# Optimization experiments

Measured on AMD Instinct MI355X. Metric: run time of the kernel, lower is better.

Reference implementation:

```python
import jax, jax.numpy as jnp
import numpy as np

N = 50000      # nodes
E = 800000     # edges (before self-loops)
IN_DIM = 128
HID = 64
OUT = 32
HEADS = 8
BN_EPS = 1e-5
NEG_SLOPE = 0.2  # PyG GATConv default


def setup_inputs() -> dict:
    key = jax.random.key(0)
    ks = jax.random.split(key, 24)
    g = lambda k, shape, fan_in: (jax.random.normal(k, shape, jnp.float32) / np.sqrt(fan_in))
    return {
        "x": jax.random.normal(ks[0], (N, IN_DIM), jnp.float32),
        "edge_index": jax.random.randint(ks[1], (2, E), 0, N, dtype=jnp.int64),
        # GCN1
        "gcn1_w": g(ks[2], (IN_DIM, HID), IN_DIM),
        "gcn1_b": jnp.zeros((HID,), jnp.float32),
        # BN1 (eval mode running stats)
        "bn1_gamma": jnp.ones((HID,), jnp.float32),
        "bn1_beta": jnp.zeros((HID,), jnp.float32),
        "bn1_mean": 0.1 * jax.random.normal(ks[3], (HID,), jnp.float32),
        "bn1_var": 0.5 + jax.random.uniform(ks[4], (HID,), jnp.float32),
        # GAT1: heads=8, per-head out=HID, concat=False -> mean over heads
        "gat1_w": g(ks[5], (HID, HEADS * HID), HID),
        "gat1_asrc": g(ks[6], (HEADS, HID), HID),
        "gat1_adst": g(ks[7], (HEADS, HID), HID),
        "gat1_b": jnp.zeros((HID,), jnp.float32),
        # GCN2
        "gcn2_w": g(ks[8], (HID, HID), HID),
        "gcn2_b": jnp.zeros((HID,), jnp.float32),
        # BN2
        "bn2_gamma": jnp.ones((HID,), jnp.float32),
        "bn2_beta": jnp.zeros((HID,), jnp.float32),
        "bn2_mean": 0.1 * jax.random.normal(ks[9], (HID,), jnp.float32),
        "bn2_var": 0.5 + jax.random.uniform(ks[10], (HID,), jnp.float32),
        # GAT2: heads=8, per-head out=OUT, concat=False
        "gat2_w": g(ks[11], (HID, HEADS * OUT), HID),
        "gat2_asrc": g(ks[12], (HEADS, OUT), OUT),
        "gat2_adst": g(ks[13], (HEADS, OUT), OUT),
        "gat2_b": jnp.zeros((OUT,), jnp.float32),
    }


def _gcn(x, src, dst, w, b, n):
    # PyG GCNConv: x @ W, symmetric norm with self-loops (src/dst already include them)
    h = x @ w
    deg = jax.ops.segment_sum(jnp.ones(src.shape[0], x.dtype), dst, num_segments=n)
    dinv = jnp.where(deg > 0, jax.lax.rsqrt(jnp.maximum(deg, 1.0)), 0.0)
    coef = dinv[src] * dinv[dst]                     # [E']
    out = jax.ops.segment_sum(coef[:, None] * h[src], dst, num_segments=n)
    return out + b


def _gat(x, src, dst, w, a_src, a_dst, b, n, heads, ch):
    # PyG GATConv (concat=False): mean over heads, softmax over incoming edges per dst
    h = (x @ w).reshape(n, heads, ch)                # [N,H,C]
    es = jnp.einsum('nhc,hc->nh', h, a_src)          # alpha_src per node
    ed = jnp.einsum('nhc,hc->nh', h, a_dst)
    e = jax.nn.leaky_relu(es[src] + ed[dst], NEG_SLOPE)  # [E',H]
    m = jax.ops.segment_max(e, dst, num_segments=n)
    m = jnp.where(jnp.isfinite(m), m, 0.0)
    ex = jnp.exp(e - m[dst])
    denom = jax.ops.segment_sum(ex, dst, num_segments=n)
    alpha = ex / (denom[dst] + 1e-16)                # [E',H]
    out = jnp.zeros((n, ch), x.dtype)
    for hd in range(heads):  # fixed small head loop keeps peak edge memory at [E',C]
        msg = alpha[:, hd, None] * h[src, hd]        # [E',C]
        out = out + jax.ops.segment_sum(msg, dst, num_segments=n)
    return out / heads + b


def _bn_eval(x, gamma, beta, mean, var):
    return (x - mean) * jax.lax.rsqrt(var + BN_EPS) * gamma + beta


def reference(x, edge_index,
              gcn1_w, gcn1_b, bn1_gamma, bn1_beta, bn1_mean, bn1_var,
              gat1_w, gat1_asrc, gat1_adst, gat1_b,
              gcn2_w, gcn2_b, bn2_gamma, bn2_beta, bn2_mean, bn2_var,
              gat2_w, gat2_asrc, gat2_adst, gat2_b):
    n = x.shape[0]
    loops = jnp.arange(n, dtype=edge_index.dtype)
    src = jnp.concatenate([edge_index[0], loops])    # self-loops (PyG default)
    dst = jnp.concatenate([edge_index[1], loops])

    h = _gcn(x, src, dst, gcn1_w, gcn1_b, n)
    h = jax.nn.relu(_bn_eval(h, bn1_gamma, bn1_beta, bn1_mean, bn1_var))
    h = jax.nn.relu(_gat(h, src, dst, gat1_w, gat1_asrc, gat1_adst, gat1_b, n, HEADS, HID))
    h = _gcn(h, src, dst, gcn2_w, gcn2_b, n)
    h = jax.nn.relu(_bn_eval(h, bn2_gamma, bn2_beta, bn2_mean, bn2_var))
    h = _gat(h, src, dst, gat2_w, gat2_asrc, gat2_adst, gat2_b, n, HEADS, OUT)
    return jax.nn.log_softmax(h, axis=1)
```

## Files before the change

### kernel.cpp

```cpp
#include <hip/hip_runtime.h>
#include <hip/hip_bf16.h>

#define NN 50000
#define NE 800000
#define IND 128
#define NH 8
#define EBLK 256
#define EPB 3125
#define NBUK 391
#define NBUKP 392
#define GH (NBUKP * EBLK)
#define PREPB 308

typedef __hip_bfloat16 bf16;
typedef __attribute__((ext_vector_type(8))) short short8;
typedef __attribute__((ext_vector_type(8))) __bf16 bf16x8;
typedef __attribute__((ext_vector_type(4))) float floatx4;
typedef __attribute__((ext_vector_type(2))) float floatx2;

static __device__ __forceinline__ short f2bf_bits(float f) {
    unsigned u = __float_as_uint(f);
    u = (u + 0x7fffu + ((u >> 16) & 1u)) >> 16;
    return (short)u;
}
static __device__ __forceinline__ float bf2f(bf16 v) { return __bfloat162float(v); }
static __device__ __forceinline__ floatx2 up2(unsigned av) {
    floatx2 r;
    r.x = __uint_as_float(av << 16);
    r.y = __uint_as_float(av & 0xffff0000u);
    return r;
}
static __device__ __forceinline__ unsigned pk2(float a, float b) {
    return (unsigned)(unsigned short)f2bf_bits(a) | ((unsigned)(unsigned short)f2bf_bits(b) << 16);
}

static __device__ __forceinline__ void scan_buckets(const int* __restrict__ bsum,
        int* sp, int* gb, int tid) {
    int v0 = (2 * tid < NBUKP) ? bsum[2 * tid] : 0;
    int v1 = (2 * tid + 1 < NBUKP) ? bsum[2 * tid + 1] : 0;
    int c = v0 + v1;
    sp[tid] = c; __syncthreads();
    int val = c;
#pragma unroll
    for (int off = 1; off < 256; off <<= 1) {
        int t = (tid >= off) ? sp[tid - off] : 0;
        __syncthreads();
        val += t; sp[tid] = val;
        __syncthreads();
    }
    int pex = val - c;
    gb[2 * tid] = pex;
    gb[2 * tid + 1] = pex + v0;
    __syncthreads();
}

__global__ __launch_bounds__(256) void bin_count_prep_kernel(const int* __restrict__ edst,
        int* __restrict__ ghist,
        const float* __restrict__ gcn1_w, const float* __restrict__ gcn2_w,
        const float* __restrict__ gat1_w, const float* __restrict__ gat2_w,
        const float* __restrict__ as1, const float* __restrict__ ad1,
        const float* __restrict__ as2, const float* __restrict__ ad2,
        bf16* __restrict__ wT1, bf16* __restrict__ wT2,
        bf16* __restrict__ wgT1, bf16* __restrict__ wgT2,
        float* __restrict__ was1, float* __restrict__ wad1,
        float* __restrict__ was2, float* __restrict__ wad2) {
    __shared__ int hsh[NBUKP];
    const int tid = threadIdx.x;
    if (blockIdx.x < EBLK) {
        const int blk = blockIdx.x;
        for (int b = tid; b < NBUKP; b += 256) hsh[b] = 0;
        __syncthreads();
        const int e0 = blk * EPB;
        for (int e = e0 + tid; e < e0 + EPB; e += 256)
            atomicAdd(&hsh[edst[e] >> 7], 1);
        __syncthreads();
        for (int b = tid; b < NBUKP; b += 256)
            ghist[b * EBLK + blk] = hsh[b];
    } else {
        int idx = (blockIdx.x - EBLK) * 256 + tid;
        if (idx < 8192) {
            int m = idx >> 7, k = idx & 127;
            ((short*)wT1)[idx] = f2bf_bits(gcn1_w[(long)k * 64 + m]);
        } else if (idx < 12288) {
            int i = idx - 8192;
            int m = i >> 6, k = i & 63;
            ((short*)wT2)[i] = f2bf_bits(gcn2_w[(long)k * 64 + m]);
        } else if (idx < 45056) {
            int i = idx - 12288;
            int m = i >> 9, k = i & 511;
            int h = k >> 6, c = k & 63;
            ((short*)wgT1)[i] = f2bf_bits(gat1_w[(long)c * 512 + h * 64 + m]);
        } else if (idx < 77824) {
            int i = idx - 45056;
            int m = i >> 9, k = i & 511;
            int h = k >> 6, c = k & 63;
            ((short*)wgT2)[i] = (m < 32) ? f2bf_bits(gat2_w[(long)c * 256 + h * 32 + m]) : (short)0;
        } else if (idx < 78336) {
            int i = idx - 77824;
            int h = i >> 6, c = i & 63;
            const float* wrow = gat1_w + (long)c * 512 + h * 64;
            float s = 0.f, d = 0.f;
            for (int cc = 0; cc < 64; ++cc) {
                float w = wrow[cc];
                s += w * as1[h * 64 + cc];
                d += w * ad1[h * 64 + cc];
            }
            was1[i] = s; wad1[i] = d;
        } else if (idx < 78848) {
            int i = idx - 78336;
            int h = i >> 6, c = i & 63;
            const float* wrow = gat2_w + (long)c * 256 + h * 32;
            float s = 0.f, d = 0.f;
            for (int cc = 0; cc < 32; ++cc) {
                float w = wrow[cc];
                s += w * as2[h * 32 + cc];
                d += w * ad2[h * 32 + cc];
            }
            was2[i] = s; wad2[i] = d;
        }
    }
}

__global__ __launch_bounds__(256) void scang1_kernel(const int* __restrict__ src,
        int* __restrict__ pre, int* __restrict__ bsum, int n) {
    __shared__ int sh[256];
    const int tid = threadIdx.x;
    const int idx = blockIdx.x * 256 + tid;
    int c = (idx < n) ? src[idx] : 0;
    sh[tid] = c; __syncthreads();
    int val = c;
#pragma unroll
    for (int off = 1; off < 256; off <<= 1) {
        int t = (tid >= off) ? sh[tid - off] : 0;
        __syncthreads();
        val += t; sh[tid] = val;
        __syncthreads();
    }
    if (idx < n) pre[idx] = val - c;
    if (tid == 255) bsum[blockIdx.x] = val;
}

__global__ __launch_bounds__(256) void bin_scatter_kernel(const int* __restrict__ esrc,
        const int* __restrict__ edst, const int* __restrict__ gpre,
        const int* __restrict__ bsum, unsigned* __restrict__ ebuf) {
    __shared__ int cur[NBUKP];
    __shared__ int sp[256], gb[512];
    const int tid = threadIdx.x, blk = blockIdx.x;
    scan_buckets(bsum, sp, gb, tid);
    for (int b = tid; b < NBUKP; b += 256)
        cur[b] = gpre[b * EBLK + blk] + gb[b];
    __syncthreads();
    const int e0 = blk * EPB;
    for (int e = e0 + tid; e < e0 + EPB; e += 256) {
        int d = edst[e], s = esrc[e];
        int pos = atomicAdd(&cur[d >> 7], 1);
        ebuf[pos] = ((unsigned)(d & 127) << 16) | (unsigned)s;
    }
}

__global__ __launch_bounds__(256) void bucket_finalize_kernel(const unsigned* __restrict__ ebuf,
        const int* __restrict__ gpre, const int* __restrict__ bsum,
        int* __restrict__ rowptr, float* __restrict__ dinv, int* __restrict__ csrc) {
    __shared__ int lh[128], lcur[128], sc[256];
    __shared__ int sp[256], gb[512];
    const int bu = blockIdx.x, tid = threadIdx.x;
    scan_buckets(bsum, sp, gb, tid);
    const int seg_beg = gpre[bu * EBLK] + gb[bu];
    const int seg_end = gpre[(bu + 1) * EBLK] + gb[bu + 1];
    if (tid < 128) lh[tid] = 0;
    __syncthreads();
    for (int i = seg_beg + tid; i < seg_end; i += 256)
        atomicAdd(&lh[ebuf[i] >> 16], 1);
    __syncthreads();
    int c = (tid < 128) ? lh[tid] : 0;
    sc[tid] = c; __syncthreads();
    int val = c;
#pragma unroll
    for (int off = 1; off < 256; off <<= 1) {
        int t = (tid >= off) ? sc[tid - off] : 0;
        __syncthreads();
        val += t; sc[tid] = val;
        __syncthreads();
    }
    int excl = val - c;
    if (tid < 128) {
        lcur[tid] = excl;
        int node = bu * 128 + tid;
        if (node < NN) {
            rowptr[node] = seg_beg + excl;
            dinv[node] = rsqrtf((float)c + 1.f);
        }
    }
    if (bu == 0 && tid == 0) rowptr[NN] = NE;
    __syncthreads();
    for (int i = seg_beg + tid; i < seg_end; i += 256) {
        unsigned u = ebuf[i];
        int pos = atomicAdd(&lcur[u >> 16], 1);
        csrc[seg_beg + pos] = (int)(u & 0xffffu);
    }
}

template<int K, int EPI, bool AF32>
__global__ __launch_bounds__(256) void mm2_kernel(const void* __restrict__ A,
        const bf16* __restrict__ wT, void* __restrict__ C,
        const float* __restrict__ bias, const float* __restrict__ rowscale,
        int nrows, int M) {
    const int row0 = blockIdx.x * 64;
    const int tid = threadIdx.x;
    const int lane = tid & 63, wave = tid >> 6;
    const int lr = lane & 15, q = lane >> 4;
    const int row = row0 + wave * 16 + lr;
    const bool rok = row < nrows;
    constexpr int NC = (EPI == 4) ? 2 : 4;
    floatx4 acc[NC] = {};
#pragma unroll 4
    for (int k0 = 0; k0 < K; k0 += 32) {
        short8 av = {0, 0, 0, 0, 0, 0, 0, 0};
        if (rok) {
            if (AF32) {
                const float* apf = (const float*)A + (long)row * K + q * 8 + k0;
                floatx4 va = *(const floatx4*)apf;
                floatx4 vb = *(const floatx4*)(apf + 4);
#pragma unroll
                for (int j = 0; j < 4; ++j) { av[j] = f2bf_bits(va[j]); av[4 + j] = f2bf_bits(vb[j]); }
            } else {
                av = *(const short8*)((const short*)A + (long)row * K + q * 8 + k0);
            }
        }
        bf16x8 a = __builtin_bit_cast(bf16x8, av);
#pragma unroll
        for (int c = 0; c < NC; ++c) {
            bf16x8 b = __builtin_bit_cast(bf16x8,
                *(const short8*)((const short*)wT + (long)(c * 16 + lr) * K + k0 + q * 8));
            acc[c] = __builtin_amdgcn_mfma_f32_16x16x32_bf16(a, b, acc[c], 0, 0, 0);
        }
    }
    if (EPI == 4) {
#pragma unroll
        for (int r = 0; r < 4; ++r) {
            int orow = row0 + wave * 16 + q * 4 + r;
            float v0 = acc[0][r] * 0.125f + bias[lr];
            float v1 = acc[1][r] * 0.125f + bias[16 + lr];
            float m = fmaxf(v0, v1);
#pragma unroll
            for (int off = 1; off < 16; off <<= 1) m = fmaxf(m, __shfl_xor(m, off));
            float s = __expf(v0 - m) + __expf(v1 - m);
#pragma unroll
            for (int off = 1; off < 16; off <<= 1) s += __shfl_xor(s, off);
            float ls = m + logf(s);
            if (orow < nrows) {
                ((float*)C)[(long)orow * 32 + lr] = v0 - ls;
                ((float*)C)[(long)orow * 32 + 16 + lr] = v1 - ls;
            }
        }
        return;
    }
#pragma unroll
    for (int c = 0; c < NC; ++c)
#pragma unroll
        for (int r = 0; r < 4; ++r) {
            int orow = row0 + wave * 16 + q * 4 + r;
            int col = c * 16 + lr;
            if (orow < nrows && col < M) {
                long o = (long)orow * M + col;
                float v = acc[c][r];
                if (EPI == 0) ((float*)C)[o] = v;
                else if (EPI == 2) {
                    v = v * 0.125f + bias[col];
                    ((bf16*)C)[o] = __float2bfloat16(fmaxf(v, 0.f));
                } else {
                    ((bf16*)C)[o] = __float2bfloat16(rowscale[orow] * v);
                }
            }
        }
}

__global__ __launch_bounds__(256) void gcn_fused_kernel(const int* __restrict__ rowptr,
        const int* __restrict__ csrc, const float* __restrict__ dinv,
        const bf16* __restrict__ hin, const float* __restrict__ b,
        const float* __restrict__ gamma, const float* __restrict__ beta,
        const float* __restrict__ mean, const float* __restrict__ var,
        bf16* __restrict__ actout) {
    const int node = blockIdx.x * 4 + (threadIdx.x >> 6);
    if (node >= NN) return;
    const int lane = threadIdx.x & 63;
    const int eslot = lane >> 5, cp = lane & 31;
    const int beg = rowptr[node], end = rowptr[node + 1];
    const int deg = end - beg;
    const float di = dinv[node];
    const char* hp = (const char*)hin + 4 * cp;
    floatx2 acc2 = {0.f, 0.f};
    const int kup = (deg + 7) & ~7;
    for (int k0 = 0; k0 < kup; k0 += 8) {
        int s_[4]; float w_[4];
#pragma unroll
        for (int u = 0; u < 4; ++u) {
            int ei = beg + k0 + 2 * u + eslot;
            int ok = ei < end;
            s_[u] = csrc[ok ? ei : beg];
            w_[u] = ok ? 1.f : 0.f;
        }
        unsigned av_[4];
#pragma unroll
        for (int u = 0; u < 4; ++u)
            av_[u] = *(const unsigned*)(hp + (long)s_[u] * 128);
#pragma unroll
        for (int u = 0; u < 4; ++u) {
            floatx2 a2 = up2(av_[u]);
            acc2 += a2 * w_[u];
        }
    }
    acc2.x += __shfl_xor(acc2.x, 32);
    acc2.y += __shfl_xor(acc2.y, 32);
    {
        unsigned sv = *(const unsigned*)(hp + (long)node * 128);
        acc2 += up2(sv);
    }
    int c0 = 2 * cp, c1 = c0 + 1;
    float x0 = acc2.x * di + b[c0];
    float x1 = acc2.y * di + b[c1];
    x0 = (x0 - mean[c0]) * rsqrtf(var[c0] + 1e-5f) * gamma[c0] + beta[c0];
    x1 = (x1 - mean[c1]) * rsqrtf(var[c1] + 1e-5f) * gamma[c1] + beta[c1];
    if (eslot == 0)
        *(unsigned*)((unsigned short*)actout + (long)node * 64 + c0) =
            pk2(fmaxf(x0, 0.f), fmaxf(x1, 0.f));
}

__global__ __launch_bounds__(256) void scores_kernel(const bf16* __restrict__ actb,
        const float* __restrict__ was, const float* __restrict__ wad,
        float* __restrict__ es, float* __restrict__ ed, int n) {
    const int node = blockIdx.x * 4 + (threadIdx.x >> 6);
    if (node >= n) return;
    const int lane = threadIdx.x & 63;
    const int h = lane >> 3, cg = lane & 7;
    short8 a8 = *(const short8*)((const short*)actb + (long)node * 64 + cg * 8);
    const float* wsp = was + h * 64 + cg * 8;
    const float* wdp = wad + h * 64 + cg * 8;
    floatx4 ws0 = *(const floatx4*)wsp, ws1 = *(const floatx4*)(wsp + 4);
    floatx4 wd0 = *(const floatx4*)wdp, wd1 = *(const floatx4*)(wdp + 4);
    float s = 0.f, d = 0.f;
#pragma unroll
    for (int j = 0; j < 4; ++j) {
        float v0 = bf2f(__builtin_bit_cast(bf16, a8[j]));
        float v1 = bf2f(__builtin_bit_cast(bf16, a8[4 + j]));
        s += v0 * ws0[j] + v1 * ws1[j];
        d += v0 * wd0[j] + v1 * wd1[j];
    }
#pragma unroll
    for (int off = 1; off < 8; off <<= 1) {
        s += __shfl_xor(s, off);
        d += __shfl_xor(d, off);
    }
    if (cg == 0) { es[node * NH + h] = s; ed[node * NH + h] = d; }
}

__global__ __launch_bounds__(256) void gat_agg_kernel(const int* __restrict__ rowptr,
        const int* __restrict__ csrc, const float* __restrict__ es, const float* __restrict__ ed,
        const bf16* __restrict__ actb, bf16* __restrict__ agg) {
    __shared__ __align__(16) float salpha[4][512];
    __shared__ int ssrcs[4][64];
    __shared__ __align__(16) float sself[4][8];
    const int wv = threadIdx.x >> 6;
    const int node = blockIdx.x * 4 + wv;
    if (node >= NN) return;
    const int lane = threadIdx.x & 63;
    const int h = lane & 7, slot = lane >> 3;
    const int beg = rowptr[node], end = rowptr[node + 1];
    const int deg = end - beg;
    const float edr = ed[node * NH + h];

    float selfe = es[node * NH + h] + edr;
    selfe = selfe > 0.f ? selfe : 0.2f * selfe;

    if (deg <= 64) {
        float ex_r[8]; int s_r[8];
        float den = 0.f;
        if (deg > 0) {
            const int dm1 = deg - 1;
#pragma unroll
            for (int b = 0; b < 8; ++b) {
                int k = b * 8 + slot;
                s_r[b] = csrc[beg + (k < deg ? k : dm1)];
            }
#pragma unroll
            for (int b = 0; b < 8; ++b) {
                float e = es[s_r[b] * NH + h] + edr;
                e = e > 0.f ? e : 0.2f * e;
                float ex = __expf(e - selfe);
                ex_r[b] = (b * 8 + slot < deg) ? ex : 0.f;
                den += ex_r[b];
            }
        }
        den += __shfl_xor(den, 8);
        den += __shfl_xor(den, 16);
        den += __shfl_xor(den, 32);
        const float invden = 1.f / (den + 1.f);

#pragma unroll
        for (int b = 0; b < 8; ++b)
            if (b * 8 < deg) salpha[wv][b * 64 + lane] = ex_r[b] * invden;
        if (h == 0) {
#pragma unroll
            for (int b = 0; b < 8; ++b)
                if (b * 8 < deg) ssrcs[wv][b * 8 + slot] = s_r[b];
        }
        if (slot == 0) sself[wv][h] = invden;

        const int hq = lane >> 5, cp = lane & 31;
        const char* actp = (const char*)actb + 4 * cp;
        const float* alp = &salpha[wv][hq * 4];
        floatx2 acc2[4] = {};
        const int kup = (deg + 3) & ~3;
        for (int k0 = 0; k0 < kup; k0 += 4) {
            int s_[4];
#pragma unroll
            for (int u = 0; u < 4; ++u) s_[u] = ssrcs[wv][k0 + u];
            unsigned av_[4];
#pragma unroll
            for (int u = 0; u < 4; ++u)
                av_[u] = *(const unsigned*)(actp + (long)s_[u] * 128);
            floatx4 al_[4];
#pragma unroll
            for (int u = 0; u < 4; ++u)
                al_[u] = *(const floatx4*)(alp + (k0 + u) * 8);
#pragma unroll
            for (int u = 0; u < 4; ++u) {
                floatx2 a2 = up2(av_[u]);
                acc2[0] += a2 * al_[u][0]; acc2[1] += a2 * al_[u][1];
                acc2[2] += a2 * al_[u][2]; acc2[3] += a2 * al_[u][3];
            }
        }
        {
            unsigned sv = *(const unsigned*)(actp + (long)node * 128);
            floatx2 a2 = up2(sv);
            floatx4 sa = *(const floatx4*)&sself[wv][hq * 4];
            acc2[0] += a2 * sa[0]; acc2[1] += a2 * sa[1];
            acc2[2] += a2 * sa[2]; acc2[3] += a2 * sa[3];
        }
#pragma unroll
        for (int j = 0; j < 4; ++j)
            *(unsigned*)((unsigned short*)agg + (long)node * 512 + (hq * 4 + j) * 64 + 2 * cp) =
                pk2(acc2[j].x, acc2[j].y);
    } else {
        float acc[NH] = {0.f, 0.f, 0.f, 0.f, 0.f, 0.f, 0.f, 0.f};
        float den = 0.f;
        for (int base = beg; base < end; base += 8) {
            int ei = base + slot;
            if (ei < end) {
                int s = csrc[ei];
                float e = es[s * NH + h] + edr;
                e = e > 0.f ? e : 0.2f * e;
                den += __expf(e - selfe);
            }
        }
        den += __shfl_xor(den, 8);
        den += __shfl_xor(den, 16);
        den += __shfl_xor(den, 32);
        const float invden = 1.f / (den + 1.f);
        for (int base = beg; base < end; base += 8) {
            int ei = base + slot;
            float al = 0.f; int sl = 0;
            if (ei < end) {
                sl = csrc[ei];
                float e = es[sl * NH + h] + edr;
                e = e > 0.f ? e : 0.2f * e;
                al = __expf(e - selfe) * invden;
            }
            salpha[wv][lane] = al;
            if (h == 0) ssrcs[wv][slot] = sl;
            int ecnt = end - base; if (ecnt > 8) ecnt = 8;
            for (int j = 0; j < ecnt; ++j) {
                int s = ssrcs[wv][j];
                float a = bf2f(actb[(long)s * 64 + lane]);
                floatx4 al0 = *(const floatx4*)&salpha[wv][j * 8];
                floatx4 al1 = *(const floatx4*)&salpha[wv][j * 8 + 4];
                acc[0] += al0[0] * a; acc[1] += al0[1] * a;
                acc[2] += al0[2] * a; acc[3] += al0[3] * a;
                acc[4] += al1[0] * a; acc[5] += al1[1] * a;
                acc[6] += al1[2] * a; acc[7] += al1[3] * a;
            }
        }
        {
            if (slot == 0) sself[wv][h] = invden;
            float a = bf2f(actb[(long)node * 64 + lane]);
            floatx4 s0 = *(const floatx4*)&sself[wv][0];
            floatx4 s1 = *(const floatx4*)&sself[wv][4];
            acc[0] += s0[0] * a; acc[1] += s0[1] * a;
            acc[2] += s0[2] * a; acc[3] += s0[3] * a;
            acc[4] += s1[0] * a; acc[5] += s1[1] * a;
            acc[6] += s1[2] * a; acc[7] += s1[3] * a;
        }
#pragma unroll
        for (int hh = 0; hh < NH; ++hh)
            agg[(long)node * 512 + hh * 64 + lane] = __float2bfloat16(acc[hh]);
    }
}

extern "C" void kernel_launch(void* const* d_in, const int* in_sizes, int n_in,
                              void* d_out, int out_size, void* d_ws, size_t ws_size,
                              hipStream_t stream) {
    const float* x        = (const float*)d_in[0];
    const int*   eidx     = (const int*)d_in[1];
    const float* gcn1_w   = (const float*)d_in[2];
    const float* gcn1_b   = (const float*)d_in[3];
    const float* bn1_g    = (const float*)d_in[4];
    const float* bn1_b    = (const float*)d_in[5];
    const float* bn1_m    = (const float*)d_in[6];
    const float* bn1_v    = (const float*)d_in[7];
    const float* gat1_w   = (const float*)d_in[8];
    const float* gat1_as  = (const float*)d_in[9];
    const float* gat1_ad  = (const float*)d_in[10];
    const float* gat1_b   = (const float*)d_in[11];
    const float* gcn2_w   = (const float*)d_in[12];
    const float* gcn2_b   = (const float*)d_in[13];
    const float* bn2_g    = (const float*)d_in[14];
    const float* bn2_b    = (const float*)d_in[15];
    const float* bn2_m    = (const float*)d_in[16];
    const float* bn2_v    = (const float*)d_in[17];
    const float* gat2_w   = (const float*)d_in[18];
    const float* gat2_as  = (const float*)d_in[19];
    const float* gat2_ad  = (const float*)d_in[20];
    const float* gat2_b   = (const float*)d_in[21];
    float* out = (float*)d_out;

    const int* esrc = eidx;
    const int* edst = eidx + NE;

    float* ws = (float*)d_ws;
    int*      ghist  = (int*)ws;
    int*      gpre   = ghist + GH;
    int*      gbsum  = gpre + GH;
    unsigned* ebuf   = (unsigned*)(gbsum + 512);
    int*      rowptr = (int*)(ebuf + NE);
    int*      csrc   = rowptr + 50048;
    float*    dinv   = (float*)(csrc + NE);
    float*    es     = dinv + 50048;
    float*    ed     = es + 400000;
    float*    was1   = ed + 400000;
    float*    wad1   = was1 + 512;
    float*    was2   = wad1 + 512;
    float*    wad2   = was2 + 512;
    bf16*     wT1    = (bf16*)(wad2 + 512);
    bf16*     wT2    = wT1 + 64 * 128;
    bf16*     wgT1   = wT2 + 64 * 64;
    bf16*     wgT2   = wgT1 + 64 * 512;
    bf16*     actb   = wgT2 + 64 * 512;
    bf16*     mmbf   = actb + (size_t)NN * 64;
    bf16*     agg    = mmbf + (size_t)NN * 64;

    auto cdiv = [](long a, long b) { return (int)((a + b - 1) / b); };
    const int GB = cdiv(NN, 64);
    const int NB = cdiv(NN, 4);

    bin_count_prep_kernel<<<EBLK + PREPB, 256, 0, stream>>>(edst, ghist,
        gcn1_w, gcn2_w, gat1_w, gat2_w, gat1_as, gat1_ad, gat2_as, gat2_ad,
        wT1, wT2, wgT1, wgT2, was1, wad1, was2, wad2);
    scang1_kernel<<<GH / 256, 256, 0, stream>>>(ghist, gpre, gbsum, GH);
    bin_scatter_kernel<<<EBLK, 256, 0, stream>>>(esrc, edst, gpre, gbsum, ebuf);
    bucket_finalize_kernel<<<NBUK, 256, 0, stream>>>(ebuf, gpre, gbsum, rowptr, dinv, csrc);

    mm2_kernel<IND, 3, true><<<GB, 256, 0, stream>>>(x, wT1, mmbf, nullptr, dinv, NN, 64);
    gcn_fused_kernel<<<NB, 256, 0, stream>>>(rowptr, csrc, dinv, mmbf,
        gcn1_b, bn1_g, bn1_b, bn1_m, bn1_v, actb);

    scores_kernel<<<NB, 256, 0, stream>>>(actb, was1, wad1, es, ed, NN);
    gat_agg_kernel<<<NB, 256, 0, stream>>>(rowptr, csrc, es, ed, actb, agg);
    mm2_kernel<512, 2, false><<<GB, 256, 0, stream>>>(agg, wgT1, actb, gat1_b, nullptr, NN, 64);

    mm2_kernel<64, 3, false><<<GB, 256, 0, stream>>>(actb, wT2, mmbf, nullptr, dinv, NN, 64);
    gcn_fused_kernel<<<NB, 256, 0, stream>>>(rowptr, csrc, dinv, mmbf,
        gcn2_b, bn2_g, bn2_b, bn2_m, bn2_v, actb);

    scores_kernel<<<NB, 256, 0, stream>>>(actb, was2, wad2, es, ed, NN);
    gat_agg_kernel<<<NB, 256, 0, stream>>>(rowptr, csrc, es, ed, actb, agg);
    mm2_kernel<512, 4, false><<<GB, 256, 0, stream>>>(agg, wgT2, out, gat2_b, nullptr, NN, 32);
}
```

Measured before the change: 378.9 us.

## Software-pipeline GAT neighbor gathers and widen GCN gather unroll

The GAT aggregation loop for low-degree nodes is restructured into 8-edge groups with two register banks. The gathers for the next group are issued before the FMAs of the current group, to overlap memory latency with compute. Score and index loads are skipped for unused 8-edge blocks instead of loading clamped duplicates. The GCN gather loop now processes 16 edges per iteration instead of 8, and both kernels switch to 32-bit unsigned address arithmetic. This trades more register pressure, and possibly lower occupancy, for more memory-level parallelism.

```diff
diff --git a/kernel.cpp b/kernel.cpp
--- a/kernel.cpp
+++ b/kernel.cpp
@@ -285,27 +285,26 @@
     if (node >= NN) return;
     const int lane = threadIdx.x & 63;
     const int eslot = lane >> 5, cp = lane & 31;
+    const unsigned cpo = 4u * (unsigned)cp;
     const int beg = rowptr[node], end = rowptr[node + 1];
-    const int deg = end - beg;
     const float di = dinv[node];
-    const char* hp = (const char*)hin + 4 * cp;
     floatx2 acc2 = {0.f, 0.f};
-    const int kup = (deg + 7) & ~7;
-    for (int k0 = 0; k0 < kup; k0 += 8) {
-        int s_[4]; float w_[4];
-#pragma unroll
-        for (int u = 0; u < 4; ++u) {
+    const int kup = ((end - beg) + 15) & ~15;
+    for (int k0 = 0; k0 < kup; k0 += 16) {
+        int s_[8]; float w_[8];
+#pragma unroll
+        for (int u = 0; u < 8; ++u) {
             int ei = beg + k0 + 2 * u + eslot;
             int ok = ei < end;
             s_[u] = csrc[ok ? ei : beg];
             w_[u] = ok ? 1.f : 0.f;
         }
-        unsigned av_[4];
-#pragma unroll
-        for (int u = 0; u < 4; ++u)
-            av_[u] = *(const unsigned*)(hp + (long)s_[u] * 128);
-#pragma unroll
-        for (int u = 0; u < 4; ++u) {
+        unsigned av_[8];
+#pragma unroll
+        for (int u = 0; u < 8; ++u)
+            av_[u] = *(const unsigned*)((const char*)hin + ((unsigned)s_[u] * 128u + cpo));
+#pragma unroll
+        for (int u = 0; u < 8; ++u) {
             floatx2 a2 = up2(av_[u]);
             acc2 += a2 * w_[u];
         }
@@ -313,7 +312,7 @@
     acc2.x += __shfl_xor(acc2.x, 32);
     acc2.y += __shfl_xor(acc2.y, 32);
     {
-        unsigned sv = *(const unsigned*)(hp + (long)node * 128);
+        unsigned sv = *(const unsigned*)((const char*)hin + ((unsigned)node * 128u + cpo));
         acc2 += up2(sv);
     }
     int c0 = 2 * cp, c1 = c0 + 1;
@@ -367,29 +366,35 @@
     const int h = lane & 7, slot = lane >> 3;
     const int beg = rowptr[node], end = rowptr[node + 1];
     const int deg = end - beg;
-    const float edr = ed[node * NH + h];
-
-    float selfe = es[node * NH + h] + edr;
+    const float edr = *(const float*)((const char*)ed + ((unsigned)node * 32u + (unsigned)h * 4u));
+
+    float selfe = *(const float*)((const char*)es + ((unsigned)node * 32u + (unsigned)h * 4u)) + edr;
     selfe = selfe > 0.f ? selfe : 0.2f * selfe;
 
     if (deg <= 64) {
+        const int nb = (deg + 7) >> 3;
+        const int dm1 = (deg > 0) ? deg - 1 : 0;
         float ex_r[8]; int s_r[8];
         float den = 0.f;
+#pragma unroll
+        for (int b = 0; b < 8; ++b) { ex_r[b] = 0.f; s_r[b] = 0; }
         if (deg > 0) {
-            const int dm1 = deg - 1;
-#pragma unroll
-            for (int b = 0; b < 8; ++b) {
-                int k = b * 8 + slot;
-                s_r[b] = csrc[beg + (k < deg ? k : dm1)];
-            }
-#pragma unroll
-            for (int b = 0; b < 8; ++b) {
-                float e = es[s_r[b] * NH + h] + edr;
-                e = e > 0.f ? e : 0.2f * e;
-                float ex = __expf(e - selfe);
-                ex_r[b] = (b * 8 + slot < deg) ? ex : 0.f;
-                den += ex_r[b];
-            }
+#pragma unroll
+            for (int b = 0; b < 8; ++b)
+                if (b < nb) {
+                    int k = b * 8 + slot;
+                    s_r[b] = csrc[beg + (k < deg ? k : dm1)];
+                }
+#pragma unroll
+            for (int b = 0; b < 8; ++b)
+                if (b < nb) {
+                    float e = *(const float*)((const char*)es +
+                              ((unsigned)s_r[b] * 32u + (unsigned)h * 4u)) + edr;
+                    e = e > 0.f ? e : 0.2f * e;
+                    float ex = __expf(e - selfe);
+                    ex_r[b] = (b * 8 + slot < deg) ? ex : 0.f;
+                    den += ex_r[b];
+                }
         }
         den += __shfl_xor(den, 8);
         den += __shfl_xor(den, 16);
@@ -398,40 +403,62 @@
 
 #pragma unroll
         for (int b = 0; b < 8; ++b)
-            if (b * 8 < deg) salpha[wv][b * 64 + lane] = ex_r[b] * invden;
+            if (b < nb) salpha[wv][b * 64 + lane] = ex_r[b] * invden;
         if (h == 0) {
 #pragma unroll
             for (int b = 0; b < 8; ++b)
-                if (b * 8 < deg) ssrcs[wv][b * 8 + slot] = s_r[b];
+                if (b < nb) ssrcs[wv][b * 8 + slot] = s_r[b];
         }
         if (slot == 0) sself[wv][h] = invden;
 
         const int hq = lane >> 5, cp = lane & 31;
-        const char* actp = (const char*)actb + 4 * cp;
-        const float* alp = &salpha[wv][hq * 4];
+        const unsigned cpo = 4u * (unsigned)cp;
         floatx2 acc2[4] = {};
-        const int kup = (deg + 3) & ~3;
-        for (int k0 = 0; k0 < kup; k0 += 4) {
-            int s_[4];
-#pragma unroll
-            for (int u = 0; u < 4; ++u) s_[u] = ssrcs[wv][k0 + u];
-            unsigned av_[4];
-#pragma unroll
-            for (int u = 0; u < 4; ++u)
-                av_[u] = *(const unsigned*)(actp + (long)s_[u] * 128);
-            floatx4 al_[4];
-#pragma unroll
-            for (int u = 0; u < 4; ++u)
-                al_[u] = *(const floatx4*)(alp + (k0 + u) * 8);
-#pragma unroll
-            for (int u = 0; u < 4; ++u) {
-                floatx2 a2 = up2(av_[u]);
-                acc2[0] += a2 * al_[u][0]; acc2[1] += a2 * al_[u][1];
-                acc2[2] += a2 * al_[u][2]; acc2[3] += a2 * al_[u][3];
-            }
+        const int ng = nb;
+        if (ng > 0) {
+            int sA0, sA1, sA2, sA3, sA4, sA5, sA6, sA7;
+            int sB0, sB1, sB2, sB3, sB4, sB5, sB6, sB7;
+            unsigned rA0, rA1, rA2, rA3, rA4, rA5, rA6, rA7;
+            unsigned rB0, rB1, rB2, rB3, rB4, rB5, rB6, rB7;
+#define LOAD_BANK(S, R, G) do { \
+    const int* sp_ = &ssrcs[wv][(G) * 8]; \
+    S##0 = sp_[0]; S##1 = sp_[1]; S##2 = sp_[2]; S##3 = sp_[3]; \
+    S##4 = sp_[4]; S##5 = sp_[5]; S##6 = sp_[6]; S##7 = sp_[7]; \
+    R##0 = *(const unsigned*)((const char*)actb + ((unsigned)S##0 * 128u + cpo)); \
+    R##1 = *(const unsigned*)((const char*)actb + ((unsigned)S##1 * 128u + cpo)); \
+    R##2 = *(const unsigned*)((const char*)actb + ((unsigned)S##2 * 128u + cpo)); \
+    R##3 = *(const unsigned*)((const char*)actb + ((unsigned)S##3 * 128u + cpo)); \
+    R##4 = *(const unsigned*)((const char*)actb + ((unsigned)S##4 * 128u + cpo)); \
+    R##5 = *(const unsigned*)((const char*)actb + ((unsigned)S##5 * 128u + cpo)); \
+    R##6 = *(const unsigned*)((const char*)actb + ((unsigned)S##6 * 128u + cpo)); \
+    R##7 = *(const unsigned*)((const char*)actb + ((unsigned)S##7 * 128u + cpo)); \
+} while (0)
+#define FMA_BANK(R, G) do { \
+    const float* ab_ = &salpha[wv][(G) * 64 + hq * 4]; \
+    unsigned rr_[8] = {R##0, R##1, R##2, R##3, R##4, R##5, R##6, R##7}; \
+    _Pragma("unroll") \
+    for (int j_ = 0; j_ < 8; ++j_) { \
+        floatx4 al_ = *(const floatx4*)(ab_ + j_ * 8); \
+        floatx2 a2_ = up2(rr_[j_]); \
+        acc2[0] += a2_ * al_[0]; acc2[1] += a2_ * al_[1]; \
+        acc2[2] += a2_ * al_[2]; acc2[3] += a2_ * al_[3]; \
+    } \
+} while (0)
+            LOAD_BANK(sA, rA, 0);
+            int g = 0;
+            while (true) {
+                if (g + 1 < ng) LOAD_BANK(sB, rB, g + 1);
+                FMA_BANK(rA, g);
+                ++g; if (g >= ng) break;
+                if (g + 1 < ng) LOAD_BANK(sA, rA, g + 1);
+                FMA_BANK(rB, g);
+                ++g; if (g >= ng) break;
+            }
+#undef LOAD_BANK
+#undef FMA_BANK
         }
         {
-            unsigned sv = *(const unsigned*)(actp + (long)node * 128);
+            unsigned sv = *(const unsigned*)((const char*)actb + ((unsigned)node * 128u + cpo));
             floatx2 a2 = up2(sv);
             floatx4 sa = *(const floatx4*)&sself[wv][hq * 4];
             acc2[0] += a2 * sa[0]; acc2[1] += a2 * sa[1];
```

New measurement: 368.2 us. 2.8% less time.
